# Performance work log

Hardware: AMD Instinct MI355X
Metric: run time of the kernel (lower is better)

The kernel has to match this reference:

```python
import jax, jax.numpy as jnp
import numpy as np

DIM = 128
P = (2, 2, 2)
D_STATE = 8
D_CONV = 4
EXPAND = 2
D_INNER = EXPAND * DIM
DT_RANK = (DIM + 15) // 16  # ceil(d_model/16) = 8
EPS = 1e-5


def setup_inputs() -> dict:
    key = jax.random.key(0)
    ks = jax.random.split(key, 8)
    B, C, Z, H, W = 2, DIM, 40, 40, 40
    s = lambda k, shape, scale: jax.random.normal(k, shape, jnp.float32) * scale
    return {
        "x": jax.random.normal(ks[0], (B, C, Z, H, W), jnp.float32),
        "norm_g": jnp.ones((C,), jnp.float32),
        "norm_b": jnp.zeros((C,), jnp.float32),
        "in_proj_w": s(ks[1], (2 * D_INNER, C), 0.02),
        "conv_w": s(ks[2], (D_INNER, D_CONV), 0.1),
        "conv_b": jnp.zeros((D_INNER,), jnp.float32),
        "x_proj_w": s(ks[3], (DT_RANK + 2 * D_STATE, D_INNER), 0.02),
        "dt_proj_w": s(ks[4], (D_INNER, DT_RANK), 0.1),
        # softplus^-1(0.01): small positive init for delta, as in mamba_ssm
        "dt_bias": jnp.log(jnp.expm1(jnp.full((D_INNER,), 0.01, jnp.float32))),
        # S4D-real init: A_log = log([1..d_state]) per channel
        "A_log": jnp.log(jnp.tile(jnp.arange(1, D_STATE + 1, dtype=jnp.float32), (D_INNER, 1))),
        "D_vec": jnp.ones((D_INNER,), jnp.float32),
        "out_proj_w": s(ks[5], (DIM, D_INNER), 0.02),
    }


def _mamba(xn, in_proj_w, conv_w, conv_b, x_proj_w, dt_proj_w, dt_bias, A_log, D_vec, out_proj_w):
    # xn: (NB, L, C)
    NB, L, _ = xn.shape
    xz = jnp.einsum('blc,ec->ble', xn, in_proj_w)          # (NB, L, 2*d_inner)
    xp, z = jnp.split(xz, 2, axis=-1)
    # causal depthwise conv1d, kernel D_CONV, truncated to L
    xpad = jnp.pad(xp, ((0, 0), (D_CONV - 1, 0), (0, 0)))
    conv = conv_b
    for k in range(D_CONV):
        conv = conv + xpad[:, k:k + L, :] * conv_w[:, k]
    u = jax.nn.silu(conv)                                  # (NB, L, d_inner)
    xdbl = jnp.einsum('bld,ed->ble', u, x_proj_w)
    dt, Bm, Cm = jnp.split(xdbl, [DT_RANK, DT_RANK + D_STATE], axis=-1)
    delta = jax.nn.softplus(jnp.einsum('blr,dr->bld', dt, dt_proj_w) + dt_bias)
    A = -jnp.exp(A_log)                                    # (d_inner, d_state)

    def step(h, inp):
        d_t, B_t, C_t, u_t = inp  # (NB,d_inner),(NB,d_state),(NB,d_state),(NB,d_inner)
        h = jnp.exp(d_t[:, :, None] * A) * h + (d_t * u_t)[:, :, None] * B_t[:, None, :]
        return h, jnp.einsum('bds,bs->bd', h, C_t)

    h0 = jnp.zeros((NB, D_INNER, D_STATE), xn.dtype)
    xs = (jnp.swapaxes(delta, 0, 1), jnp.swapaxes(Bm, 0, 1),
          jnp.swapaxes(Cm, 0, 1), jnp.swapaxes(u, 0, 1))
    _, ys = jax.lax.scan(step, h0, xs)                     # ys: (L, NB, d_inner)
    y = jnp.swapaxes(ys, 0, 1) + u * D_vec
    y = y * jax.nn.silu(z)
    return jnp.einsum('bld,cd->blc', y, out_proj_w)        # (NB, L, C)


def reference(x, norm_g, norm_b, in_proj_w, conv_w, conv_b, x_proj_w, dt_proj_w,
              dt_bias, A_log, D_vec, out_proj_w):
    B, C, Z, H, W = x.shape
    p1, p2, p3 = P
    NZ, NH, NW = Z // p1, H // p2, W // p3
    NB, L = B * p1 * p2 * p3, NZ * NH * NW
    # patch reshuffle: (B,C,Z,H,W) -> (B*p1*p2*p3, C, NZ, NH, NW)
    xd = x.reshape(B, C, NZ, p1, NH, p2, NW, p3).transpose(0, 3, 5, 7, 1, 2, 4, 6)
    xf = jnp.swapaxes(xd.reshape(NB, C, L), 1, 2)          # (NB, L, C)
    # LayerNorm over channel dim
    mu = xf.mean(-1, keepdims=True)
    var = xf.var(-1, keepdims=True)
    xn = (xf - mu) * jax.lax.rsqrt(var + EPS) * norm_g + norm_b
    yo = _mamba(xn, in_proj_w, conv_w, conv_b, x_proj_w, dt_proj_w, dt_bias,
                A_log, D_vec, out_proj_w)                  # (NB, L, C)
    # undo reshuffle
    xo = jnp.swapaxes(yo, 1, 2).reshape(B, p1, p2, p3, C, NZ, NH, NW)
    xo = xo.transpose(0, 4, 5, 1, 6, 2, 7, 3).reshape(B, C, Z, H, W)
    return xo + x
```

## Files before the change

### kernel.cpp

```cpp
#include <hip/hip_runtime.h>

#define NBATCH 16
#define LSEQ   8000
#define MROWS  128000
#define CDIM   128
#define DI     256
#define DS     8
#define DTR    8
#define NXP    24
#define NC     250
#define CL     32

#define OFF_PB    0ull
#define OFF_XN    1024000ull
#define OFF_STA   1024000ull
#define OFF_XP    33792000ull
#define OFF_XDBL  33792000ull
#define OFF_STH   46080000ull
#define OFF_ZS    99328000ull
#define OFF_U     164864000ull
#define WS_NEEDED 230400000ull

#define P_G    0
#define P_B    128
#define P_IPW  256
#define P_CW   65792
#define P_CB   66816
#define P_XPW  67072
#define P_DTW  73216
#define P_DTB  75264
#define P_ALOG 75520
#define P_DVEC 77568
#define P_OPW  77824
#define P_TOT  110592

typedef __attribute__((ext_vector_type(8))) short bf16x8;
typedef __attribute__((ext_vector_type(4))) float f32x4;
typedef __attribute__((ext_vector_type(2))) float f32x2;

__device__ __forceinline__ float bf2f(unsigned short a) {
    union { unsigned int u; float f; } v; v.u = ((unsigned int)a) << 16; return v.f;
}
__device__ __forceinline__ unsigned short f2bf(float f) {
    union { float f; unsigned int u; } v; v.f = f;
    unsigned int r = v.u + 0x7FFFu + ((v.u >> 16) & 1u);
    return (unsigned short)(r >> 16);
}
__device__ __forceinline__ unsigned short f2bf_cvt(float f) {
    unsigned int r;
    asm("v_cvt_pk_bf16_f32 %0, %1, %2" : "=v"(r) : "v"(f), "v"(0.f));
    return (unsigned short)r;
}
__device__ __forceinline__ bool bfmode(const void* g) {
    return ((const unsigned int*)g)[0] == 0x3F803F80u;
}
__device__ __forceinline__ float rd(const void* p, size_t i, bool bf) {
    return bf ? bf2f(((const unsigned short*)p)[i]) : ((const float*)p)[i];
}
__device__ __forceinline__ f32x2 pk_fma(f32x2 a, f32x2 b, f32x2 c) {
    f32x2 d;
    asm("v_pk_fma_f32 %0, %1, %2, %3" : "=v"(d) : "v"(a), "v"(b), "v"(c));
    return d;
}
__device__ __forceinline__ f32x2 pk_mul(f32x2 a, f32x2 b) {
    f32x2 d;
    asm("v_pk_mul_f32 %0, %1, %2" : "=v"(d) : "v"(a), "v"(b));
    return d;
}
__device__ __forceinline__ int m_of(int b, int sp) {
    int z = sp / 1600;
    int rem = sp - z * 1600;
    int h = rem / 40;
    int w = rem - h * 40;
    int nb = b * 8 + (z & 1) * 4 + (h & 1) * 2 + (w & 1);
    int l = (z >> 1) * 400 + (h >> 1) * 20 + (w >> 1);
    return nb * LSEQ + l;
}

__global__ __launch_bounds__(256) void param_convert(const void* g, const void* b, const void* ipw,
                                                     const void* cw, const void* cb, const void* xpw,
                                                     const void* dtw, const void* dtb, const void* alog,
                                                     const void* dvec, const void* opw,
                                                     unsigned short* __restrict__ pb)
{
    int gid = blockIdx.x * 256 + threadIdx.x;
    if (gid >= P_TOT) return;
    bool bf = bfmode(g);
    const void* src; int off;
    if      (gid < P_B)    { src = g;    off = P_G; }
    else if (gid < P_IPW)  { src = b;    off = P_B; }
    else if (gid < P_CW)   { src = ipw;  off = P_IPW; }
    else if (gid < P_CB)   { src = cw;   off = P_CW; }
    else if (gid < P_XPW)  { src = cb;   off = P_CB; }
    else if (gid < P_DTW)  { src = xpw;  off = P_XPW; }
    else if (gid < P_DTB)  { src = dtw;  off = P_DTW; }
    else if (gid < P_ALOG) { src = dtb;  off = P_DTB; }
    else if (gid < P_DVEC) { src = alog; off = P_ALOG; }
    else if (gid < P_OPW)  { src = dvec; off = P_DVEC; }
    else                   { src = opw;  off = P_OPW; }
    pb[gid] = f2bf(rd(src, gid - off, bf));
}

__global__ __launch_bounds__(256) void lnorm_kernel(const void* __restrict__ x,
                                                    const unsigned short* __restrict__ pb,
                                                    unsigned short* __restrict__ xn)
{
    __shared__ float tile[128][65];
    __shared__ float psum[4][64], psqs[4][64];
    __shared__ float smu[64], srs[64];
    int b  = blockIdx.y;
    int sp0 = blockIdx.x * 64;
    int t = threadIdx.x;

    int spi = t & 63, cpart = t >> 6;
    const float* xf = (const float*)x;
#pragma unroll
    for (int pass = 0; pass < 32; ++pass) {
        int c = pass * 4 + cpart;
        tile[c][spi] = xf[((size_t)b * CDIM + c) * 64000 + sp0 + spi];
    }
    __syncthreads();

    {
        float s = 0.f, ss = 0.f;
        int c0 = cpart * 32;
#pragma unroll
        for (int cc = 0; cc < 32; ++cc) {
            float v = tile[c0 + cc][spi];
            s += v; ss += v * v;
        }
        psum[cpart][spi] = s; psqs[cpart][spi] = ss;
    }
    __syncthreads();
    if (cpart == 0) {
        float s  = psum[0][spi] + psum[1][spi] + psum[2][spi] + psum[3][spi];
        float ss = psqs[0][spi] + psqs[1][spi] + psqs[2][spi] + psqs[3][spi];
        float m = s * (1.f / CDIM);
        float var = ss * (1.f / CDIM) - m * m;
        smu[spi] = m;
        srs[spi] = rsqrtf(var + 1e-5f);
    }
    __syncthreads();

    int c = t & 127, half = t >> 7;
    float gc = bf2f(pb[P_G + c]), bc = bf2f(pb[P_B + c]);
#pragma unroll
    for (int pass = 0; pass < 32; ++pass) {
        int j = pass * 2 + half;
        int m = m_of(b, sp0 + j);
        float v = (tile[c][j] - smu[j]) * srs[j] * gc + bc;
        xn[(size_t)m * CDIM + c] = f2bf(v);
    }
}

__global__ __launch_bounds__(256) void gemm_bt_kernel(const unsigned short* __restrict__ A,
                                                      const unsigned short* __restrict__ W,
                                                      void* __restrict__ D,
                                                      int K, int Nact, int ldd, int act)
{
    __shared__ unsigned short As[128 * 32];
    __shared__ unsigned short Ws[128 * 32];
    int tid = threadIdx.x;
    int m0 = blockIdx.x * 128;
    int n0 = blockIdx.y * 128;
    int wave = tid >> 6, lane = tid & 63;
    int wm = (wave & 1) * 64, wn = (wave >> 1) * 64;
    int lrow = lane & 15, lk = (lane >> 4) * 8;
    int quad = lane >> 4;

    f32x4 acc[4][4];
#pragma unroll
    for (int i = 0; i < 4; i++)
#pragma unroll
        for (int j = 0; j < 4; j++) acc[i][j] = (f32x4){0.f, 0.f, 0.f, 0.f};

    int rowA0 = tid >> 2, kcA0 = (tid & 3) << 3;
    int rowA1 = (tid + 256) >> 2, kcA1 = (tid & 3) << 3;

    for (int kt = 0; kt < K; kt += 32) {
        *(uint4*)&As[rowA0 * 32 + kcA0] = *(const uint4*)&A[(size_t)(m0 + rowA0) * K + kt + kcA0];
        *(uint4*)&As[rowA1 * 32 + kcA1] = *(const uint4*)&A[(size_t)(m0 + rowA1) * K + kt + kcA1];
        uint4 z4 = {0u, 0u, 0u, 0u};
        uint4 w0 = (n0 + rowA0 < Nact) ? *(const uint4*)&W[(size_t)(n0 + rowA0) * K + kt + kcA0] : z4;
        uint4 w1 = (n0 + rowA1 < Nact) ? *(const uint4*)&W[(size_t)(n0 + rowA1) * K + kt + kcA1] : z4;
        *(uint4*)&Ws[rowA0 * 32 + kcA0] = w0;
        *(uint4*)&Ws[rowA1 * 32 + kcA1] = w1;
        __syncthreads();

        bf16x8 af[4], bfr[4];
#pragma unroll
        for (int i = 0; i < 4; i++) af[i]  = *(const bf16x8*)&As[(wm + i * 16 + lrow) * 32 + lk];
#pragma unroll
        for (int j = 0; j < 4; j++) bfr[j] = *(const bf16x8*)&Ws[(wn + j * 16 + lrow) * 32 + lk];
#pragma unroll
        for (int i = 0; i < 4; i++)
#pragma unroll
            for (int j = 0; j < 4; j++)
                acc[i][j] = __builtin_amdgcn_mfma_f32_16x16x32_bf16(af[i], bfr[j], acc[i][j], 0, 0, 0);
        __syncthreads();
    }

#pragma unroll
    for (int i = 0; i < 4; i++)
#pragma unroll
        for (int j = 0; j < 4; j++) {
            int n = n0 + wn + j * 16 + lrow;
            if (n < Nact) {
#pragma unroll
                for (int r = 0; r < 4; r++) {
                    int m = m0 + wm + i * 16 + quad * 4 + r;
                    float v = acc[i][j][r];
                    if (act == 2) {
                        ((float*)D)[(size_t)m * ldd + n] = v;
                    } else {
                        if (act == 1) v = v / (1.f + __expf(-v));
                        ((unsigned short*)D)[(size_t)m * ldd + n] = f2bf(v);
                    }
                }
            }
        }
}

__global__ __launch_bounds__(256) void gemm_conv_kernel(const unsigned short* __restrict__ A,
                                                        const unsigned short* __restrict__ W,
                                                        const unsigned short* __restrict__ cw,
                                                        const unsigned short* __restrict__ cb,
                                                        unsigned short* __restrict__ u)
{
    __shared__ unsigned short As[128 * 32];
    __shared__ unsigned short Ws[128 * 32];
    __shared__ unsigned short Dt[128 * 132];

    int tid = threadIdx.x;
    int tile = blockIdx.x & 63;
    int nb = blockIdx.x >> 6;
    int n0 = blockIdx.y * 128;
    int m0 = nb * 8000 + tile * 125;
    int mA = m0 - 3;
    int wave = tid >> 6, lane = tid & 63;
    int wm = (wave & 1) * 64, wn = (wave >> 1) * 64;
    int lrow = lane & 15, lk = (lane >> 4) * 8;
    int quad = lane >> 4;

    f32x4 acc[4][4];
#pragma unroll
    for (int i = 0; i < 4; i++)
#pragma unroll
        for (int j = 0; j < 4; j++) acc[i][j] = (f32x4){0.f, 0.f, 0.f, 0.f};

    int rowA0 = tid >> 2, kcA0 = (tid & 3) << 3;
    int rowA1 = (tid + 256) >> 2;

    for (int kt = 0; kt < CDIM; kt += 32) {
        uint4 z4 = {0u, 0u, 0u, 0u};
        uint4 a0 = (tile == 0 && rowA0 < 3) ? z4
                 : *(const uint4*)&A[(size_t)(mA + rowA0) * CDIM + kt + kcA0];
        uint4 a1 = *(const uint4*)&A[(size_t)(mA + rowA1) * CDIM + kt + kcA0];
        *(uint4*)&As[rowA0 * 32 + kcA0] = a0;
        *(uint4*)&As[rowA1 * 32 + kcA0] = a1;
        *(uint4*)&Ws[rowA0 * 32 + kcA0] = *(const uint4*)&W[(size_t)(n0 + rowA0) * CDIM + kt + kcA0];
        *(uint4*)&Ws[rowA1 * 32 + kcA0] = *(const uint4*)&W[(size_t)(n0 + rowA1) * CDIM + kt + kcA0];
        __syncthreads();

        bf16x8 af[4], bfr[4];
#pragma unroll
        for (int i = 0; i < 4; i++) af[i]  = *(const bf16x8*)&As[(wm + i * 16 + lrow) * 32 + lk];
#pragma unroll
        for (int j = 0; j < 4; j++) bfr[j] = *(const bf16x8*)&Ws[(wn + j * 16 + lrow) * 32 + lk];
#pragma unroll
        for (int i = 0; i < 4; i++)
#pragma unroll
            for (int j = 0; j < 4; j++)
                acc[i][j] = __builtin_amdgcn_mfma_f32_16x16x32_bf16(af[i], bfr[j], acc[i][j], 0, 0, 0);
        __syncthreads();
    }

#pragma unroll
    for (int i = 0; i < 4; i++)
#pragma unroll
        for (int j = 0; j < 4; j++) {
            int nl = wn + j * 16 + lrow;
            int tr = wm + i * 16 + quad * 4;
            unsigned int c01, c23;
            asm("v_cvt_pk_bf16_f32 %0, %1, %2" : "=v"(c01) : "v"(acc[i][j][0]), "v"(acc[i][j][1]));
            asm("v_cvt_pk_bf16_f32 %0, %1, %2" : "=v"(c23) : "v"(acc[i][j][2]), "v"(acc[i][j][3]));
            *(unsigned int*)&Dt[nl * 132 + tr]     = c01;
            *(unsigned int*)&Dt[nl * 132 + tr + 2] = c23;
        }
    __syncthreads();

    {
        int nl = tid & 127, half = tid >> 7;
        int dch = n0 + nl;
        float cw0 = bf2f(cw[dch * 4 + 0]), cw1 = bf2f(cw[dch * 4 + 1]);
        float cw2 = bf2f(cw[dch * 4 + 2]), cw3 = bf2f(cw[dch * 4 + 3]);
        float cbv = bf2f(cb[dch]);
        int tr0 = half ? 66 : 3;
        int nsteps = half ? 62 : 63;
        const unsigned short* col = &Dt[nl * 132];
        float x0 = bf2f(col[tr0 - 3]), x1 = bf2f(col[tr0 - 2]), x2 = bf2f(col[tr0 - 1]);
        unsigned short* uout = &u[(size_t)(m0 + tr0 - 3) * DI + dch];
#pragma unroll 1
        for (int k = 0; k < nsteps; ++k) {
            float x3 = bf2f(col[tr0 + k]);
            float a = cbv + cw0 * x0 + cw1 * x1 + cw2 * x2 + cw3 * x3;
            float uv = a * __builtin_amdgcn_rcpf(1.f + __expf(-a));
            *uout = f2bf_cvt(uv);
            uout += DI;
            x0 = x1; x1 = x2; x2 = x3;
        }
    }
}


#define BODY1(UR, RO) do {                                                       \
    union { f32x4 q; f32x2 h[2]; } qa, qb, qc, qd;                               \
    qa.q = *(const f32x4*)(rfp + (RO));                                          \
    qb.q = *(const f32x4*)(rfp + (RO) + 4);                                      \
    qc.q = *(const f32x4*)(rfp + (RO) + 8);                                      \
    qd.q = *(const f32x4*)(rfp + (RO) + 12);                                     \
    f32x2 din2 = pk_fma(qa.h[0], Wq[0], bias2);                                  \
    din2 = pk_fma(qa.h[1], Wq[1], din2);                                         \
    din2 = pk_fma(qb.h[0], Wq[2], din2);                                         \
    din2 = pk_fma(qb.h[1], Wq[3], din2);                                         \
    float din = din2.x + din2.y;                                                 \
    float e = __expf(din);                                                       \
    float w = 1.f + e;                                                           \
    float p1 = __builtin_amdgcn_rcpf(w);                                         \
    float delta = (din > 15.f) ? din : __logf(w);                                \
    float du = delta * bf2f(UR);                                                 \
    float p2 = p1 * p1;                                                          \
    f32x2 q1; q1.x = p1; q1.y = p2;                                              \
    f32x2 pp2; pp2.x = p2; pp2.y = p2;                                           \
    f32x2 q2 = pk_mul(q1, pp2);                                                  \
    f32x2 pp4; pp4.x = q2.y; pp4.y = q2.y;                                       \
    f32x2 q3 = pk_mul(q1, pp4);                                                  \
    f32x2 q4 = pk_mul(q2, pp4);                                                  \
    f32x2 du2; du2.x = du; du2.y = du;                                           \
    h2[0] = pk_fma(du2, qc.h[0], pk_mul(q1, h2[0]));                             \
    h2[1] = pk_fma(du2, qc.h[1], pk_mul(q2, h2[1]));                             \
    h2[2] = pk_fma(du2, qd.h[0], pk_mul(q3, h2[2]));                             \
    h2[3] = pk_fma(du2, qd.h[1], pk_mul(q4, h2[3]));                             \
    P *= p1;                                                                     \
} while (0)

__global__ __launch_bounds__(256) void scan_phase1(const unsigned short* __restrict__ u,
                                                   const float* __restrict__ xdbl,
                                                   const unsigned short* __restrict__ dtw,
                                                   const unsigned short* __restrict__ dtb,
                                                   const unsigned short* __restrict__ alog,
                                                   float* __restrict__ stA, float* __restrict__ stH)
{
    __shared__ float xs[CL * NXP];
    int c = blockIdx.x, nb = blockIdx.y, d = threadIdx.x;
    size_t base = (size_t)nb * LSEQ + (size_t)c * CL;
    {
        const uint4* src = (const uint4*)(xdbl + base * NXP);
        uint4* dst = (uint4*)xs;
        int tt = threadIdx.x;
        if (tt < 192) dst[tt] = src[tt];
    }
    float Av[DS];
    f32x2 Wq[4];
#pragma unroll
    for (int r = 0; r < 4; r++) {
        Wq[r].x = bf2f(dtw[d * DTR + 2 * r]);
        Wq[r].y = bf2f(dtw[d * DTR + 2 * r + 1]);
    }
#pragma unroll
    for (int s = 0; s < DS; s++) Av[s] = -__expf(bf2f(alog[d * DS + s]));
    float A1 = Av[0];
    bool fast = (A1 == -1.0f);
#pragma unroll
    for (int s = 1; s < DS; s++)
        fast = fast && (fabsf(Av[s] - (float)(s + 1) * A1) <= 0.02f * (float)(s + 1) * fabsf(A1));
    float bias = bf2f(dtb[d]);
    f32x2 bias2; bias2.x = bias; bias2.y = 0.f;
    size_t o = (((size_t)c * NBATCH + nb) * DI + d) * DS;
    const unsigned short* up = u + base * DI + d;
    __syncthreads();

    if (fast) {
        f32x2 h2[4];
#pragma unroll
        for (int i = 0; i < 4; i++) { h2[i].x = 0.f; h2[i].y = 0.f; }
        float P = 1.f;
        const float* rfp = xs;
        unsigned short u0 = up[0], u1 = up[DI];
        const unsigned short* uld = up + 2 * DI;
#pragma unroll 1
        for (int t = 0; t < CL - 2; t += 2) {
            unsigned short ua = uld[0], ub = uld[DI]; uld += 2 * DI;
            BODY1(u0, 0);
            BODY1(u1, NXP);
            u0 = ua; u1 = ub;
            rfp += 2 * NXP;
        }
        BODY1(u0, 0);
        BODY1(u1, NXP);
        float P2 = P * P, P3 = P2 * P, P4 = P2 * P2;
        float apv[DS] = {P, P2, P3, P4, P4 * P, P3 * P3, P4 * P3, P4 * P4};
#pragma unroll
        for (int s = 0; s < DS; s++) stA[o + s] = apv[s];
#pragma unroll
        for (int i = 0; i < 4; i++) { stH[o + 2 * i] = h2[i].x; stH[o + 2 * i + 1] = h2[i].y; }
    } else {
        float Wdt[DTR];
#pragma unroll
        for (int r = 0; r < 4; r++) { Wdt[2 * r] = Wq[r].x; Wdt[2 * r + 1] = Wq[r].y; }
        float h[DS], ap[DS];
#pragma unroll
        for (int s = 0; s < DS; s++) { h[s] = 0.f; ap[s] = 1.f; }
        const float* rfp = xs;
        const unsigned short* uld = up;
#pragma unroll 1
        for (int t = 0; t < CL; ++t) {
            float uv = bf2f(*uld); uld += DI;
            float din = bias;
#pragma unroll
            for (int r = 0; r < DTR; r++) din += rfp[r] * Wdt[r];
            float delta = (din > 15.f) ? din : __logf(1.f + __expf(din));
            float du = delta * uv;
#pragma unroll
            for (int s = 0; s < DS; s++) {
                float dA = __expf(delta * Av[s]);
                h[s] = dA * h[s] + du * rfp[8 + s];
                ap[s] *= dA;
            }
            rfp += NXP;
        }
#pragma unroll
        for (int s = 0; s < DS; s++) { stA[o + s] = ap[s]; stH[o + s] = h[s]; }
    }
}

__global__ __launch_bounds__(256) void scan_phase2(float* __restrict__ stA, float* __restrict__ stH)
{
    size_t t = blockIdx.x * 256 + threadIdx.x;
    const size_t stride = (size_t)NBATCH * DI * DS;
    float hin = 0.f;
    size_t idx = t;
    float a[10], hl[10], an[10], hn[10];
#pragma unroll
    for (int j = 0; j < 10; ++j) { a[j] = stA[idx + j * stride]; hl[j] = stH[idx + j * stride]; }
#pragma unroll 1
    for (int g = 0; g < 25; ++g) {
        size_t nidx = idx + 10 * stride;
        if (g < 24) {
#pragma unroll
            for (int j = 0; j < 10; ++j) { an[j] = stA[nidx + j * stride]; hn[j] = stH[nidx + j * stride]; }
        }
#pragma unroll
        for (int j = 0; j < 10; ++j) {
            stH[idx + j * stride] = hin;
            hin = a[j] * hin + hl[j];
        }
#pragma unroll
        for (int j = 0; j < 10; ++j) { a[j] = an[j]; hl[j] = hn[j]; }
        idx = nidx;
    }
}

#define BODY3(UR, ZR, RO, ZO) do {                                               \
    union { f32x4 q; f32x2 h[2]; } qa, qb, qc, qd, qe, qf;                       \
    qa.q = *(const f32x4*)(rfp + (RO));                                          \
    qb.q = *(const f32x4*)(rfp + (RO) + 4);                                      \
    qc.q = *(const f32x4*)(rfp + (RO) + 8);                                      \
    qd.q = *(const f32x4*)(rfp + (RO) + 12);                                     \
    qe.q = *(const f32x4*)(rfp + (RO) + 16);                                     \
    qf.q = *(const f32x4*)(rfp + (RO) + 20);                                     \
    f32x2 din2 = pk_fma(qa.h[0], Wq[0], bias2);                                  \
    din2 = pk_fma(qa.h[1], Wq[1], din2);                                         \
    din2 = pk_fma(qb.h[0], Wq[2], din2);                                         \
    din2 = pk_fma(qb.h[1], Wq[3], din2);                                         \
    float din = din2.x + din2.y;                                                 \
    float e = __expf(din);                                                       \
    float w = 1.f + e;                                                           \
    float p1 = __builtin_amdgcn_rcpf(w);                                         \
    float delta = (din > 15.f) ? din : __logf(w);                                \
    float uv = bf2f(UR);                                                         \
    float du = delta * uv;                                                       \
    float p2 = p1 * p1;                                                          \
    f32x2 q1; q1.x = p1; q1.y = p2;                                              \
    f32x2 pp2; pp2.x = p2; pp2.y = p2;                                           \
    f32x2 q2 = pk_mul(q1, pp2);                                                  \
    f32x2 pp4; pp4.x = q2.y; pp4.y = q2.y;                                       \
    f32x2 q3 = pk_mul(q1, pp4);                                                  \
    f32x2 q4 = pk_mul(q2, pp4);                                                  \
    f32x2 du2; du2.x = du; du2.y = du;                                           \
    h2[0] = pk_fma(du2, qc.h[0], pk_mul(q1, h2[0]));                             \
    h2[1] = pk_fma(du2, qc.h[1], pk_mul(q2, h2[1]));                             \
    h2[2] = pk_fma(du2, qd.h[0], pk_mul(q3, h2[2]));                             \
    h2[3] = pk_fma(du2, qd.h[1], pk_mul(q4, h2[3]));                             \
    f32x2 y2v = pk_mul(h2[0], qe.h[0]);                                          \
    y2v = pk_fma(h2[1], qe.h[1], y2v);                                           \
    y2v = pk_fma(h2[2], qf.h[0], y2v);                                           \
    y2v = pk_fma(h2[3], qf.h[1], y2v);                                           \
    float y = __builtin_fmaf(uv, Dv, y2v.x) + y2v.y;                             \
    zw[ZO] = f2bf_cvt(y * bf2f(ZR));                                             \
} while (0)

__global__ __launch_bounds__(256) void scan_phase3(unsigned short* __restrict__ zs,
                                                   const unsigned short* __restrict__ u,
                                                   const float* __restrict__ xdbl,
                                                   const unsigned short* __restrict__ dtw,
                                                   const unsigned short* __restrict__ dtb,
                                                   const unsigned short* __restrict__ alog,
                                                   const unsigned short* __restrict__ dvec,
                                                   const float* __restrict__ stH)
{
    __shared__ float xs[CL * NXP];
    int c = blockIdx.x, nb = blockIdx.y, d = threadIdx.x;
    size_t base = (size_t)nb * LSEQ + (size_t)c * CL;
    {
        const uint4* src = (const uint4*)(xdbl + base * NXP);
        uint4* dst = (uint4*)xs;
        int tt = threadIdx.x;
        if (tt < 192) dst[tt] = src[tt];
    }
    float Av[DS];
    f32x2 Wq[4];
#pragma unroll
    for (int r = 0; r < 4; r++) {
        Wq[r].x = bf2f(dtw[d * DTR + 2 * r]);
        Wq[r].y = bf2f(dtw[d * DTR + 2 * r + 1]);
    }
#pragma unroll
    for (int s = 0; s < DS; s++) Av[s] = -__expf(bf2f(alog[d * DS + s]));
    float A1 = Av[0];
    bool fast = (A1 == -1.0f);
#pragma unroll
    for (int s = 1; s < DS; s++)
        fast = fast && (fabsf(Av[s] - (float)(s + 1) * A1) <= 0.02f * (float)(s + 1) * fabsf(A1));
    float bias = bf2f(dtb[d]);
    f32x2 bias2; bias2.x = bias; bias2.y = 0.f;
    float Dv = bf2f(dvec[d]);
    size_t o = (((size_t)c * NBATCH + nb) * DI + d) * DS;
    const unsigned short* up = u + base * DI + d;
    unsigned short* zp = zs + base * DI + d;
    __syncthreads();

    if (fast) {
        f32x2 h2[4];
#pragma unroll
        for (int i = 0; i < 4; i++) { h2[i].x = stH[o + 2 * i]; h2[i].y = stH[o + 2 * i + 1]; }
        const float* rfp = xs;
        unsigned short u0 = up[0], u1 = up[DI];
        unsigned short z0 = zp[0], z1 = zp[DI];
        const unsigned short* uld = up + 2 * DI;
        const unsigned short* zld = zp + 2 * DI;
        unsigned short* zw = zp;
#pragma unroll 1
        for (int t = 0; t < CL - 2; t += 2) {
            unsigned short ua = uld[0], ub = uld[DI]; uld += 2 * DI;
            unsigned short za = zld[0], zb = zld[DI]; zld += 2 * DI;
            BODY3(u0, z0, 0, 0);
            BODY3(u1, z1, NXP, DI);
            u0 = ua; u1 = ub; z0 = za; z1 = zb;
            zw += 2 * DI; rfp += 2 * NXP;
        }
        BODY3(u0, z0, 0, 0);
        BODY3(u1, z1, NXP, DI);
    } else {
        float Wdt[DTR];
#pragma unroll
        for (int r = 0; r < 4; r++) { Wdt[2 * r] = Wq[r].x; Wdt[2 * r + 1] = Wq[r].y; }
        float h[DS];
#pragma unroll
        for (int s = 0; s < DS; s++) h[s] = stH[o + s];
        const float* rfp = xs;
        const unsigned short* uld = up;
        unsigned short* zw = zp;
#pragma unroll 1
        for (int t = 0; t < CL; ++t) {
            float uv = bf2f(*uld); uld += DI;
            float szv = bf2f(*zw);
            float din = bias;
#pragma unroll
            for (int r = 0; r < DTR; r++) din += rfp[r] * Wdt[r];
            float delta = (din > 15.f) ? din : __logf(1.f + __expf(din));
            float du = delta * uv;
            float y = 0.f;
#pragma unroll
            for (int s = 0; s < DS; s++) {
                float dA = __expf(delta * Av[s]);
                h[s] = dA * h[s] + du * rfp[8 + s];
                y += h[s] * rfp[16 + s];
            }
            y += uv * Dv;
            *zw = f2bf(y * szv);
            zw += DI;
            rfp += NXP;
        }
    }
}

__global__ __launch_bounds__(256) void unpatch_kernel(const void* __restrict__ x,
                                                      const unsigned short* __restrict__ y2,
                                                      float* __restrict__ out)
{
    __shared__ float ytile[64][129];
    int b  = blockIdx.y;
    int sp0 = blockIdx.x * 64;
    int t = threadIdx.x;

    {
        int c = t & 127, half = t >> 7;
#pragma unroll
        for (int pass = 0; pass < 32; ++pass) {
            int j = pass * 2 + half;
            int m = m_of(b, sp0 + j);
            ytile[j][c] = bf2f(y2[(size_t)m * CDIM + c]);
        }
    }
    __syncthreads();

    const float* xf = (const float*)x;
    int spi = t & 63, cpart = t >> 6;
#pragma unroll
    for (int pass = 0; pass < 32; ++pass) {
        int c = pass * 4 + cpart;
        size_t idx = ((size_t)b * CDIM + c) * 64000 + sp0 + spi;
        out[idx] = xf[idx] + ytile[spi][c];
    }
}

extern "C" void kernel_launch(void* const* d_in, const int* in_sizes, int n_in,
                              void* d_out, int out_size, void* d_ws, size_t ws_size,
                              hipStream_t stream)
{
    const void* x     = d_in[0];
    const void* ng    = d_in[1];
    const void* nb_   = d_in[2];
    const void* ipw   = d_in[3];
    const void* cw    = d_in[4];
    const void* cb    = d_in[5];
    const void* xpw   = d_in[6];
    const void* dtw   = d_in[7];
    const void* dtb   = d_in[8];
    const void* alog  = d_in[9];
    const void* dvec  = d_in[10];
    const void* opw   = d_in[11];
    float* out = (float*)d_out;

    if (ws_size < WS_NEEDED) return;

    char* ws = (char*)d_ws;
    unsigned short* pb   = (unsigned short*)(ws + OFF_PB);
    unsigned short* xn   = (unsigned short*)(ws + OFF_XN);
    float* stA = (float*)(ws + OFF_STA);
    float* stH = (float*)(ws + OFF_STH);
    float* xdblf = (float*)(ws + OFF_XDBL);
    unsigned short* zs   = (unsigned short*)(ws + OFF_ZS);
    unsigned short* u    = (unsigned short*)(ws + OFF_U);
    unsigned short* y2   = xn;

    param_convert<<<432, 256, 0, stream>>>(ng, nb_, ipw, cw, cb, xpw, dtw, dtb, alog, dvec, opw, pb);
    lnorm_kernel<<<dim3(1000, 2), 256, 0, stream>>>(x, pb, xn);
    gemm_conv_kernel<<<dim3(1024, 2), 256, 0, stream>>>(xn, pb + P_IPW, pb + P_CW, pb + P_CB, u);
    gemm_bt_kernel<<<dim3(1000, 2), 256, 0, stream>>>(xn, pb + P_IPW + 256 * 128, zs, CDIM, DI, DI, 1);
    gemm_bt_kernel<<<dim3(1000, 1), 256, 0, stream>>>(u, pb + P_XPW, xdblf, DI, NXP, NXP, 2);
    scan_phase1<<<dim3(NC, NBATCH), 256, 0, stream>>>(u, xdblf, pb + P_DTW, pb + P_DTB, pb + P_ALOG,
                                                      stA, stH);
    scan_phase2<<<128, 256, 0, stream>>>(stA, stH);
    scan_phase3<<<dim3(NC, NBATCH), 256, 0, stream>>>(zs, u, xdblf, pb + P_DTW, pb + P_DTB,
                                                      pb + P_ALOG, pb + P_DVEC, stH);
    gemm_bt_kernel<<<dim3(1000, 1), 256, 0, stream>>>(zs, pb + P_OPW, y2, DI, CDIM, CDIM, 0);
    unpatch_kernel<<<dim3(1000, 2), 256, 0, stream>>>(x, y2, out);
}
```

Baseline: 410.2 us.

## Fuse x_proj GEMM with scan phase 1 using the xdbl tile kept in LDS

The x_proj GEMM and the first chunked-scan phase are merged into one kernel. Each 128-row block computes its xdbl tile with MFMA, writes it to global memory for phase 3, and also keeps it in LDS, then runs the phase-1 chunk scan over four 32-step chunks. This removes one kernel launch and the global re-read of xdbl by phase 1. In exchange, grid parallelism for the scan drops from 4000 blocks to 1000, each doing four chunks serially. The GEMM stores to LDS (128x24 floats) add shared-memory pressure.

Result: faster. 398.6 us (-2.8%).

```diff
diff --git a/kernel.cpp b/kernel.cpp
--- a/kernel.cpp
+++ b/kernel.cpp
@@ -210,12 +210,8 @@
                 for (int r = 0; r < 4; r++) {
                     int m = m0 + wm + i * 16 + quad * 4 + r;
                     float v = acc[i][j][r];
-                    if (act == 2) {
-                        ((float*)D)[(size_t)m * ldd + n] = v;
-                    } else {
-                        if (act == 1) v = v / (1.f + __expf(-v));
-                        ((unsigned short*)D)[(size_t)m * ldd + n] = f2bf(v);
-                    }
+                    if (act == 1) v = v / (1.f + __expf(-v));
+                    ((unsigned short*)D)[(size_t)m * ldd + n] = f2bf(v);
                 }
             }
         }
@@ -344,29 +340,81 @@
     P *= p1;                                                                     \
 } while (0)
 
-__global__ __launch_bounds__(256) void scan_phase1(const unsigned short* __restrict__ u,
-                                                   const float* __restrict__ xdbl,
-                                                   const unsigned short* __restrict__ dtw,
-                                                   const unsigned short* __restrict__ dtb,
-                                                   const unsigned short* __restrict__ alog,
-                                                   float* __restrict__ stA, float* __restrict__ stH)
-{
-    __shared__ float xs[CL * NXP];
-    int c = blockIdx.x, nb = blockIdx.y, d = threadIdx.x;
-    size_t base = (size_t)nb * LSEQ + (size_t)c * CL;
-    {
-        const uint4* src = (const uint4*)(xdbl + base * NXP);
-        uint4* dst = (uint4*)xs;
-        int tt = threadIdx.x;
-        if (tt < 192) dst[tt] = src[tt];
-    }
-    float Av[DS];
+__global__ __launch_bounds__(256) void gemm_xdbl_scan1(const unsigned short* __restrict__ u,
+                                                       const unsigned short* __restrict__ W,
+                                                       const unsigned short* __restrict__ dtw,
+                                                       const unsigned short* __restrict__ dtb,
+                                                       const unsigned short* __restrict__ alog,
+                                                       float* __restrict__ xdbl,
+                                                       float* __restrict__ stA,
+                                                       float* __restrict__ stH)
+{
+    __shared__ unsigned short As[128 * 32];
+    __shared__ unsigned short Ws[128 * 32];
+    __shared__ float Dxs[128 * NXP];
+    int tid = threadIdx.x;
+    int m0 = blockIdx.x * 128;
+    int wave = tid >> 6, lane = tid & 63;
+    int wm = (wave & 1) * 64, wn = (wave >> 1) * 64;
+    int lrow = lane & 15, lk = (lane >> 4) * 8;
+    int quad = lane >> 4;
+
+    f32x4 acc[4][4];
+#pragma unroll
+    for (int i = 0; i < 4; i++)
+#pragma unroll
+        for (int j = 0; j < 4; j++) acc[i][j] = (f32x4){0.f, 0.f, 0.f, 0.f};
+
+    int rowA0 = tid >> 2, kcA0 = (tid & 3) << 3;
+    int rowA1 = (tid + 256) >> 2;
+
+    for (int kt = 0; kt < DI; kt += 32) {
+        *(uint4*)&As[rowA0 * 32 + kcA0] = *(const uint4*)&u[(size_t)(m0 + rowA0) * DI + kt + kcA0];
+        *(uint4*)&As[rowA1 * 32 + kcA0] = *(const uint4*)&u[(size_t)(m0 + rowA1) * DI + kt + kcA0];
+        uint4 z4 = {0u, 0u, 0u, 0u};
+        uint4 w0 = (rowA0 < NXP) ? *(const uint4*)&W[(size_t)rowA0 * DI + kt + kcA0] : z4;
+        *(uint4*)&Ws[rowA0 * 32 + kcA0] = w0;
+        *(uint4*)&Ws[rowA1 * 32 + kcA0] = z4;
+        __syncthreads();
+
+        bf16x8 af[4], bfr[4];
+#pragma unroll
+        for (int i = 0; i < 4; i++) af[i]  = *(const bf16x8*)&As[(wm + i * 16 + lrow) * 32 + lk];
+#pragma unroll
+        for (int j = 0; j < 4; j++) bfr[j] = *(const bf16x8*)&Ws[(wn + j * 16 + lrow) * 32 + lk];
+#pragma unroll
+        for (int i = 0; i < 4; i++)
+#pragma unroll
+            for (int j = 0; j < 4; j++)
+                acc[i][j] = __builtin_amdgcn_mfma_f32_16x16x32_bf16(af[i], bfr[j], acc[i][j], 0, 0, 0);
+        __syncthreads();
+    }
+
+#pragma unroll
+    for (int i = 0; i < 4; i++)
+#pragma unroll
+        for (int j = 0; j < 4; j++) {
+            int n = wn + j * 16 + lrow;
+            if (n < NXP) {
+#pragma unroll
+                for (int r = 0; r < 4; r++) {
+                    int ml = wm + i * 16 + quad * 4 + r;
+                    float v = acc[i][j][r];
+                    xdbl[(size_t)(m0 + ml) * NXP + n] = v;
+                    Dxs[ml * NXP + n] = v;
+                }
+            }
+        }
+    __syncthreads();
+
+    int d = tid;
     f32x2 Wq[4];
 #pragma unroll
     for (int r = 0; r < 4; r++) {
         Wq[r].x = bf2f(dtw[d * DTR + 2 * r]);
         Wq[r].y = bf2f(dtw[d * DTR + 2 * r + 1]);
     }
+    float Av[DS];
 #pragma unroll
     for (int s = 0; s < DS; s++) Av[s] = -__expf(bf2f(alog[d * DS + s]));
     float A1 = Av[0];
@@ -376,61 +424,66 @@
         fast = fast && (fabsf(Av[s] - (float)(s + 1) * A1) <= 0.02f * (float)(s + 1) * fabsf(A1));
     float bias = bf2f(dtb[d]);
     f32x2 bias2; bias2.x = bias; bias2.y = 0.f;
-    size_t o = (((size_t)c * NBATCH + nb) * DI + d) * DS;
-    const unsigned short* up = u + base * DI + d;
-    __syncthreads();
-
-    if (fast) {
-        f32x2 h2[4];
-#pragma unroll
-        for (int i = 0; i < 4; i++) { h2[i].x = 0.f; h2[i].y = 0.f; }
-        float P = 1.f;
-        const float* rfp = xs;
-        unsigned short u0 = up[0], u1 = up[DI];
-        const unsigned short* uld = up + 2 * DI;
+
 #pragma unroll 1
-        for (int t = 0; t < CL - 2; t += 2) {
-            unsigned short ua = uld[0], ub = uld[DI]; uld += 2 * DI;
+    for (int k = 0; k < 4; ++k) {
+        int gm0 = m0 + 32 * k;
+        int nb = gm0 / 8000;
+        int cc = (gm0 - nb * 8000) >> 5;
+        size_t o = (((size_t)cc * NBATCH + nb) * DI + d) * DS;
+        const unsigned short* up = u + (size_t)gm0 * DI + d;
+        const float* rfp = &Dxs[32 * k * NXP];
+
+        if (fast) {
+            f32x2 h2[4];
+#pragma unroll
+            for (int i = 0; i < 4; i++) { h2[i].x = 0.f; h2[i].y = 0.f; }
+            float P = 1.f;
+            unsigned short u0 = up[0], u1 = up[DI];
+            const unsigned short* uld = up + 2 * DI;
+#pragma unroll 1
+            for (int t = 0; t < CL - 2; t += 2) {
+                unsigned short ua = uld[0], ub = uld[DI]; uld += 2 * DI;
+                BODY1(u0, 0);
+                BODY1(u1, NXP);
+                u0 = ua; u1 = ub;
+                rfp += 2 * NXP;
+            }
             BODY1(u0, 0);
             BODY1(u1, NXP);
-            u0 = ua; u1 = ub;
-            rfp += 2 * NXP;
-        }
-        BODY1(u0, 0);
-        BODY1(u1, NXP);
-        float P2 = P * P, P3 = P2 * P, P4 = P2 * P2;
-        float apv[DS] = {P, P2, P3, P4, P4 * P, P3 * P3, P4 * P3, P4 * P4};
-#pragma unroll
-        for (int s = 0; s < DS; s++) stA[o + s] = apv[s];
-#pragma unroll
-        for (int i = 0; i < 4; i++) { stH[o + 2 * i] = h2[i].x; stH[o + 2 * i + 1] = h2[i].y; }
-    } else {
-        float Wdt[DTR];
-#pragma unroll
-        for (int r = 0; r < 4; r++) { Wdt[2 * r] = Wq[r].x; Wdt[2 * r + 1] = Wq[r].y; }
-        float h[DS], ap[DS];
-#pragma unroll
-        for (int s = 0; s < DS; s++) { h[s] = 0.f; ap[s] = 1.f; }
-        const float* rfp = xs;
-        const unsigned short* uld = up;
+            float P2 = P * P, P3 = P2 * P, P4 = P2 * P2;
+            float apv[DS] = {P, P2, P3, P4, P4 * P, P3 * P3, P4 * P3, P4 * P4};
+#pragma unroll
+            for (int s = 0; s < DS; s++) stA[o + s] = apv[s];
+#pragma unroll
+            for (int i = 0; i < 4; i++) { stH[o + 2 * i] = h2[i].x; stH[o + 2 * i + 1] = h2[i].y; }
+        } else {
+            float Wdt[DTR];
+#pragma unroll
+            for (int r = 0; r < 4; r++) { Wdt[2 * r] = Wq[r].x; Wdt[2 * r + 1] = Wq[r].y; }
+            float h[DS], ap[DS];
+#pragma unroll
+            for (int s = 0; s < DS; s++) { h[s] = 0.f; ap[s] = 1.f; }
+            const unsigned short* uld = up;
 #pragma unroll 1
-        for (int t = 0; t < CL; ++t) {
-            float uv = bf2f(*uld); uld += DI;
-            float din = bias;
-#pragma unroll
-            for (int r = 0; r < DTR; r++) din += rfp[r] * Wdt[r];
-            float delta = (din > 15.f) ? din : __logf(1.f + __expf(din));
-            float du = delta * uv;
-#pragma unroll
-            for (int s = 0; s < DS; s++) {
-                float dA = __expf(delta * Av[s]);
-                h[s] = dA * h[s] + du * rfp[8 + s];
-                ap[s] *= dA;
+            for (int t = 0; t < CL; ++t) {
+                float uv = bf2f(*uld); uld += DI;
+                float din = bias;
+#pragma unroll
+                for (int r = 0; r < DTR; r++) din += rfp[r] * Wdt[r];
+                float delta = (din > 15.f) ? din : __logf(1.f + __expf(din));
+                float du = delta * uv;
+#pragma unroll
+                for (int s = 0; s < DS; s++) {
+                    float dA = __expf(delta * Av[s]);
+                    h[s] = dA * h[s] + du * rfp[8 + s];
+                    ap[s] *= dA;
+                }
+                rfp += NXP;
             }
-            rfp += NXP;
-        }
-#pragma unroll
-        for (int s = 0; s < DS; s++) { stA[o + s] = ap[s]; stH[o + s] = h[s]; }
+#pragma unroll
+            for (int s = 0; s < DS; s++) { stA[o + s] = ap[s]; stH[o + s] = h[s]; }
+        }
     }
 }
 
@@ -659,9 +712,8 @@
     lnorm_kernel<<<dim3(1000, 2), 256, 0, stream>>>(x, pb, xn);
     gemm_conv_kernel<<<dim3(1024, 2), 256, 0, stream>>>(xn, pb + P_IPW, pb + P_CW, pb + P_CB, u);
     gemm_bt_kernel<<<dim3(1000, 2), 256, 0, stream>>>(xn, pb + P_IPW + 256 * 128, zs, CDIM, DI, DI, 1);
-    gemm_bt_kernel<<<dim3(1000, 1), 256, 0, stream>>>(u, pb + P_XPW, xdblf, DI, NXP, NXP, 2);
-    scan_phase1<<<dim3(NC, NBATCH), 256, 0, stream>>>(u, xdblf, pb + P_DTW, pb + P_DTB, pb + P_ALOG,
-                                                      stA, stH);
+    gemm_xdbl_scan1<<<dim3(1000, 1), 256, 0, stream>>>(u, pb + P_XPW, pb + P_DTW, pb + P_DTB,
+                                                       pb + P_ALOG, xdblf, stA, stH);
     scan_phase2<<<128, 256, 0, stream>>>(stA, stH);
     scan_phase3<<<dim3(NC, NBATCH), 256, 0, stream>>>(zs, u, xdblf, pb + P_DTW, pb + P_DTB,
                                                       pb + P_ALOG, pb + P_DVEC, stH);
```
